# Kernel optimization log

Hardware: AMD Instinct MI355X
Metric: run time of the kernel (lower is better)

The kernel has to match this reference:

```python
import jax, jax.numpy as jnp
import numpy as np

N_NODES = 100000
N_EDGES = 1200000
D_IN = 64
D_HID = 64
BN_EPS = 1e-5


def setup_inputs() -> dict:
    key = jax.random.key(0)
    ks = jax.random.split(key, 16)
    x = jax.random.normal(ks[0], (N_NODES, D_IN), dtype=jnp.float32)
    edge_index = jax.random.randint(ks[1], (2, N_EDGES), 0, N_NODES, dtype=jnp.int64)
    s = 1.0 / np.sqrt(D_HID)
    W1 = jax.random.uniform(ks[2], (D_IN, D_HID), jnp.float32, -s, s)
    b1 = jax.random.uniform(ks[3], (D_HID,), jnp.float32, -s, s)
    W2 = jax.random.uniform(ks[4], (D_HID, D_HID), jnp.float32, -s, s)
    b2 = jax.random.uniform(ks[5], (D_HID,), jnp.float32, -s, s)
    W3 = jax.random.uniform(ks[6], (D_HID, D_HID), jnp.float32, -s, s)
    b3 = jax.random.uniform(ks[7], (D_HID,), jnp.float32, -s, s)
    gamma1 = jnp.ones((D_HID,), jnp.float32)
    beta1 = jnp.zeros((D_HID,), jnp.float32)
    gamma2 = jnp.ones((D_HID,), jnp.float32)
    beta2 = jnp.zeros((D_HID,), jnp.float32)
    return {"x": x, "edge_index": edge_index, "batch_size": 1,
            "W1": W1, "b1": b1, "gamma1": gamma1, "beta1": beta1,
            "W2": W2, "b2": b2, "gamma2": gamma2, "beta2": beta2,
            "W3": W3, "b3": b3}


def _gcn_norm(edge_index, n):
    # PyG GCNConv: add self-loops, symmetric normalization D^-1/2 (A+I) D^-1/2
    loop = jnp.arange(n, dtype=edge_index.dtype)
    src = jnp.concatenate([edge_index[0], loop])
    dst = jnp.concatenate([edge_index[1], loop])
    deg = jax.ops.segment_sum(jnp.ones_like(dst, dtype=jnp.float32), dst, num_segments=n)
    dinv = jnp.where(deg > 0, jax.lax.rsqrt(jnp.maximum(deg, 1.0)), 0.0)
    norm = dinv[src] * dinv[dst]  # [E + N]
    return src, dst, norm


def _gcn_conv(h, W, b, src, dst, norm, n):
    h = h @ W                      # [N, D]
    msg = h[src] * norm[:, None]   # gather + scale, [E+N, D]
    out = jax.ops.segment_sum(msg, dst, num_segments=n)  # scatter-add
    return out + b


def _bn_train(h, gamma, beta):
    # BatchNorm1d over nodes, training-mode (biased batch statistics)
    m = h.mean(axis=0)
    v = h.var(axis=0)
    return (h - m) * jax.lax.rsqrt(v + BN_EPS) * gamma + beta


def reference(x, edge_index, batch_size,
              W1, b1, gamma1, beta1, W2, b2, gamma2, beta2, W3, b3):
    n = x.shape[0]
    src, dst, norm = _gcn_norm(edge_index, n)
    h = _gcn_conv(x, W1, b1, src, dst, norm, n)
    h = jax.nn.relu(_bn_train(h, gamma1, beta1))
    h = _gcn_conv(h, W2, b2, src, dst, norm, n)
    h = jax.nn.relu(_bn_train(h, gamma2, beta2))
    h = _gcn_conv(h, W3, b3, src, dst, norm, n)
    return h  # output_type == 'hidden'
```

## Files before the change

kernel.cpp:

```cpp
#include <hip/hip_runtime.h>
#include <hip/hip_bf16.h>

#define D 64

typedef __attribute__((ext_vector_type(8))) short bf16x8;
typedef __attribute__((ext_vector_type(8))) unsigned short u16x8;
typedef __attribute__((ext_vector_type(4))) float f32x4;

__device__ __forceinline__ short f2bf(float x) {
    unsigned u = __float_as_uint(x);
    unsigned r = (u + 0x7fffu + ((u >> 16) & 1u)) >> 16;
    return (short)r;
}
__device__ __forceinline__ float bf2f(unsigned short u) {
    return __uint_as_float((unsigned)u << 16);
}

__global__ void detect_kernel(const unsigned int* e32, int* flag) {
    __shared__ int nz;
    if (threadIdx.x == 0) nz = 0;
    __syncthreads();
    if (e32[2 * threadIdx.x + 1] != 0) nz = 1;
    __syncthreads();
    if (threadIdx.x == 0) *flag = (nz == 0) ? 1 : 0;
}

__device__ __forceinline__ int load_idx(const void* e, int is64, long long i) {
    if (is64) return (int)((const long long*)e)[i];
    return ((const int*)e)[i];
}

#define NBLK 256

__global__ __launch_bounds__(256) void bucket_count_kernel(
    const void* edges, const int* flag, int* pbh, int E, int shift) {
    __shared__ int h[512];
    for (int i = threadIdx.x; i < 512; i += 256) h[i] = 0;
    __syncthreads();
    int is64 = *flag;
    int chunk = (E + gridDim.x - 1) / gridDim.x;
    int s0 = blockIdx.x * chunk;
    int s1 = min(E, s0 + chunk);
    for (int e = s0 + (int)threadIdx.x; e < s1; e += 256) {
        int d = load_idx(edges, is64, (long long)E + e);
        atomicAdd(&h[d >> shift], 1);
    }
    __syncthreads();
    for (int i = threadIdx.x; i < 512; i += 256) pbh[blockIdx.x * 512 + i] = h[i];
}

__global__ __launch_bounds__(256) void colscan_kernel(int* pbh, int* btot) {
    int b = blockIdx.x;
    int k = threadIdx.x;
    __shared__ int sA[256], sB[256];
    int v = pbh[k * 512 + b];
    sA[k] = v;
    __syncthreads();
    int* src = sA;
    int* dst = sB;
    for (int d = 1; d < 256; d <<= 1) {
        dst[k] = src[k] + (k >= d ? src[k - d] : 0);
        __syncthreads();
        int* t = src; src = dst; dst = t;
    }
    pbh[k * 512 + b] = src[k] - v;
    if (k == 255) btot[b] = src[255];
}

__global__ __launch_bounds__(512) void basescan_kernel(const int* btot, int* bbase, int E) {
    __shared__ int sA[512], sB[512];
    int b = threadIdx.x;
    int v = btot[b];
    sA[b] = v;
    __syncthreads();
    int* src = sA;
    int* dst = sB;
    for (int d = 1; d < 512; d <<= 1) {
        dst[b] = src[b] + (b >= d ? src[b - d] : 0);
        __syncthreads();
        int* t = src; src = dst; dst = t;
    }
    bbase[b] = src[b] - v;
    if (b == 0) bbase[512] = E;
}

__global__ __launch_bounds__(256) void bucket_scatter_kernel(
    const void* edges, const int* flag, const int* pbh, const int* bbase,
    unsigned* staging, int E, int shift) {
    __shared__ int cur[512];
    for (int i = threadIdx.x; i < 512; i += 256)
        cur[i] = pbh[blockIdx.x * 512 + i] + bbase[i];
    __syncthreads();
    int is64 = *flag;
    int chunk = (E + gridDim.x - 1) / gridDim.x;
    int s0 = blockIdx.x * chunk;
    int s1 = min(E, s0 + chunk);
    unsigned mask = (unsigned)((1 << shift) - 1);
    for (int e = s0 + (int)threadIdx.x; e < s1; e += 256) {
        int s = load_idx(edges, is64, e);
        int d = load_idx(edges, is64, (long long)E + e);
        int b = d >> shift;
        int pos = atomicAdd(&cur[b], 1);
        staging[pos] = ((unsigned)s << shift) | ((unsigned)d & mask);
    }
}

__global__ __launch_bounds__(256) void bucket_fill_kernel(
    const unsigned* __restrict__ staging, const int* __restrict__ bbase,
    int* __restrict__ offs, float* __restrict__ dinv, int* __restrict__ srcs,
    int shift, int n, int E) {
    int b = blockIdx.x;
    int bstart = bbase[b], bend = bbase[b + 1];
    int bsz = 1 << shift;
    unsigned mask = (unsigned)(bsz - 1);
    int v0 = b << shift;
    int nloc = min(bsz, n - v0);

    __shared__ int cnt[512], cur[512], sA[512], sB[512];
    for (int i = threadIdx.x; i < bsz; i += 256) cnt[i] = 0;
    __syncthreads();
    for (int idx = bstart + (int)threadIdx.x; idx < bend; idx += 256)
        atomicAdd(&cnt[staging[idx] & mask], 1);
    __syncthreads();
    for (int i = threadIdx.x; i < bsz; i += 256) sA[i] = cnt[i];
    __syncthreads();
    int* src = sA;
    int* dst = sB;
    for (int d = 1; d < bsz; d <<= 1) {
        for (int i = threadIdx.x; i < bsz; i += 256)
            dst[i] = src[i] + (i >= d ? src[i - d] : 0);
        __syncthreads();
        int* t = src; src = dst; dst = t;
    }
    for (int i = threadIdx.x; i < bsz; i += 256) {
        int excl = src[i] - cnt[i];
        cur[i] = excl;
        if (i < nloc) {
            offs[v0 + i] = bstart + excl;
            dinv[v0 + i] = rsqrtf((float)(cnt[i] + 1));
        }
    }
    if (b == 0 && threadIdx.x == 0) offs[n] = E;
    __syncthreads();
    for (int idx = bstart + (int)threadIdx.x; idx < bend; idx += 256) {
        unsigned u = staging[idx];
        int ld = (int)(u & mask);
        int pos = atomicAdd(&cur[ld], 1);
        srcs[bstart + pos] = (int)(u >> shift);
    }
}

__global__ __launch_bounds__(256) void mm_bn_kernel(
    const float* __restrict__ Xf, const unsigned short* __restrict__ Xb, int x_is_bf16,
    const float* __restrict__ W,
    const float* __restrict__ stats, const float* __restrict__ gamma,
    const float* __restrict__ beta, int use_bn, float inv_n,
    const float* __restrict__ dinv,
    unsigned short* __restrict__ Y, int n) {
    int lane = threadIdx.x & 63;
    int m = lane & 15;
    int quad = lane >> 4;

    float sc[16], sh[16];
#pragma unroll
    for (int s = 0; s < 2; s++) {
#pragma unroll
        for (int j = 0; j < 8; j++) {
            float scale = 1.f, shift = 0.f;
            if (use_bn) {
                int f = s * 32 + quad * 8 + j;
                float mean = stats[f] * inv_n;
                float var = stats[64 + f] * inv_n - mean * mean;
                float rs = rsqrtf(var + 1e-5f);
                scale = rs * gamma[f];
                shift = beta[f] - mean * scale;
            }
            sc[s * 8 + j] = scale;
            sh[s * 8 + j] = shift;
        }
    }

    bf16x8 bfrag[4][2];
#pragma unroll
    for (int nt = 0; nt < 4; nt++) {
#pragma unroll
        for (int s = 0; s < 2; s++) {
#pragma unroll
            for (int j = 0; j < 8; j++) {
                int k = s * 32 + quad * 8 + j;
                bfrag[nt][s][j] = f2bf(W[k * 64 + nt * 16 + m]);
            }
        }
    }

    int wave = blockIdx.x * 4 + (threadIdx.x >> 6);
    int nwaves = gridDim.x * 4;
    int ntiles = (n + 15) >> 4;
    const f32x4 zero = {0.f, 0.f, 0.f, 0.f};

    for (int t = wave; t < ntiles; t += nwaves) {
        int r = t * 16 + m;
        if (r >= n) r = n - 1;
        float av[16];
        if (x_is_bf16) {
            const unsigned short* xr = Xb + (long long)r * 64;
            u16x8 u0 = *(const u16x8*)(xr + quad * 8);
            u16x8 u1 = *(const u16x8*)(xr + 32 + quad * 8);
#pragma unroll
            for (int j = 0; j < 8; j++) {
                av[j] = bf2f(u0[j]);
                av[8 + j] = bf2f(u1[j]);
            }
        } else {
            const float* xr = Xf + (long long)r * 64;
            f32x4 a0 = *(const f32x4*)(xr + quad * 8);
            f32x4 a1 = *(const f32x4*)(xr + quad * 8 + 4);
            f32x4 a2 = *(const f32x4*)(xr + 32 + quad * 8);
            f32x4 a3 = *(const f32x4*)(xr + 32 + quad * 8 + 4);
#pragma unroll
            for (int j = 0; j < 4; j++) {
                av[j] = a0[j];
                av[4 + j] = a1[j];
                av[8 + j] = a2[j];
                av[12 + j] = a3[j];
            }
        }
        bf16x8 A0, A1;
#pragma unroll
        for (int j = 0; j < 8; j++) {
            float v0 = av[j] * sc[j] + sh[j];
            float v1 = av[8 + j] * sc[8 + j] + sh[8 + j];
            if (use_bn) {
                v0 = fmaxf(v0, 0.f);
                v1 = fmaxf(v1, 0.f);
            }
            A0[j] = f2bf(v0);
            A1[j] = f2bf(v1);
        }

        f32x4 acc[4];
#pragma unroll
        for (int nt = 0; nt < 4; nt++) {
            acc[nt] = __builtin_amdgcn_mfma_f32_16x16x32_bf16(A0, bfrag[nt][0], zero, 0, 0, 0);
            acc[nt] = __builtin_amdgcn_mfma_f32_16x16x32_bf16(A1, bfrag[nt][1], acc[nt], 0, 0, 0);
        }

        int row0 = t * 16 + quad * 4;
        float dv[4];
#pragma unroll
        for (int i = 0; i < 4; i++) {
            int rr = row0 + i;
            dv[i] = (rr < n) ? dinv[rr] : 0.f;
        }
#pragma unroll
        for (int nt = 0; nt < 4; nt++) {
#pragma unroll
            for (int i = 0; i < 4; i++) {
                int rr = row0 + i;
                if (rr < n)
                    Y[(long long)rr * 64 + nt * 16 + m] = (unsigned short)f2bf(acc[nt][i] * dv[i]);
            }
        }
    }
}

__global__ __launch_bounds__(256) void agg_kernel(const unsigned short* __restrict__ T,
                                                  const int* __restrict__ offs,
                                                  const int* __restrict__ srcs,
                                                  const float* __restrict__ dinv,
                                                  const float* __restrict__ bias,
                                                  unsigned short* __restrict__ out16,
                                                  float* __restrict__ out32, int out_bf16,
                                                  int n) {
    int v = blockIdx.x * 4 + (threadIdx.x >> 6);
    if (v >= n) return;
    int lane = threadIdx.x & 63;
    float acc = bf2f(T[(long long)v * D + lane]);
    int j = offs[v], j1 = offs[v + 1];
    for (; j + 8 <= j1; j += 8) {
        int sidx[8];
#pragma unroll
        for (int u = 0; u < 8; u++) sidx[u] = srcs[j + u];
        float t[8];
#pragma unroll
        for (int u = 0; u < 8; u++) t[u] = bf2f(T[(long long)sidx[u] * D + lane]);
        acc += ((t[0] + t[1]) + (t[2] + t[3])) + ((t[4] + t[5]) + (t[6] + t[7]));
    }
    if (j < j1) {
        int sidx[8];
        float wgt[8];
#pragma unroll
        for (int u = 0; u < 8; u++) {
            int jj = j + u;
            int jc = jj < j1 ? jj : j1 - 1;
            sidx[u] = srcs[jc];
            wgt[u] = (jj < j1) ? 1.f : 0.f;
        }
        float t[8];
#pragma unroll
        for (int u = 0; u < 8; u++) t[u] = bf2f(T[(long long)sidx[u] * D + lane]);
        float p0 = wgt[0] * t[0] + wgt[1] * t[1];
        float p1 = wgt[2] * t[2] + wgt[3] * t[3];
        float p2 = wgt[4] * t[4] + wgt[5] * t[5];
        float p3 = wgt[6] * t[6] + wgt[7] * t[7];
        acc += (p0 + p1) + (p2 + p3);
    }
    float val = dinv[v] * acc + bias[lane];
    if (out_bf16)
        out16[(long long)v * D + lane] = (unsigned short)f2bf(val);
    else
        out32[(long long)v * D + lane] = val;
}

__global__ __launch_bounds__(256) void bnstats_kernel(const unsigned short* __restrict__ H,
                                                      float* __restrict__ stats, int n) {
    int f = threadIdx.x & 63;
    int r = threadIdx.x >> 6;
    float s = 0.f, q = 0.f;
    for (int node = blockIdx.x * 4 + r; node < n; node += gridDim.x * 4) {
        float x = bf2f(H[(long long)node * D + f]);
        s += x;
        q += x * x;
    }
    __shared__ float ls[256], lq[256];
    ls[threadIdx.x] = s;
    lq[threadIdx.x] = q;
    __syncthreads();
    if (r == 0) {
        s = ls[f] + ls[64 + f] + ls[128 + f] + ls[192 + f];
        q = lq[f] + lq[64 + f] + lq[128 + f] + lq[192 + f];
        atomicAdd(&stats[f], s);
        atomicAdd(&stats[64 + f], q);
    }
}

extern "C" void kernel_launch(void* const* d_in, const int* in_sizes, int n_in,
                              void* d_out, int out_size, void* d_ws, size_t ws_size,
                              hipStream_t stream) {
    const float* x = (const float*)d_in[0];
    const void* edges = d_in[1];
    const float* W1 = (const float*)d_in[3];
    const float* b1 = (const float*)d_in[4];
    const float* gamma1 = (const float*)d_in[5];
    const float* beta1 = (const float*)d_in[6];
    const float* W2 = (const float*)d_in[7];
    const float* b2 = (const float*)d_in[8];
    const float* gamma2 = (const float*)d_in[9];
    const float* beta2 = (const float*)d_in[10];
    const float* W3 = (const float*)d_in[11];
    const float* b3 = (const float*)d_in[12];

    const int N = in_sizes[0] / D;
    const int E = in_sizes[1] / 2;
    const float inv_n = 1.f / (float)N;

    int shift = 8;
    while ((((long long)N - 1) >> shift) + 1 > 512) shift++;
    const int nbuk = (int)(((long long)N - 1) >> shift) + 1;

    char* ws = (char*)d_ws;
    size_t off = 0;
    auto alloc = [&](size_t bytes) -> void* {
        void* p = ws + off;
        off = (off + bytes + 255) & ~(size_t)255;
        return p;
    };
    float*    dinv    = (float*)   alloc((size_t)N * 4);
    int*      offs    = (int*)     alloc((size_t)(N + 1) * 4);
    int*      srcs    = (int*)     alloc((size_t)E * 4);
    unsigned* staging = (unsigned*)alloc((size_t)E * 4);
    int*      pbh     = (int*)     alloc((size_t)NBLK * 512 * 4);
    int*      btot    = (int*)     alloc(512 * 4);
    int*      bbase   = (int*)     alloc(513 * 4);
    int*      flag    = (int*)     alloc(4);
    float*    stats   = (float*)   alloc(256 * 4);
    unsigned short* bufA = (unsigned short*)alloc((size_t)N * D * 2);
    unsigned short* hbuf = (unsigned short*)alloc((size_t)N * D * 2);
    float*    outf    = (float*)d_out;

    const int aggb = (N + 3) / 4;

    detect_kernel<<<1, 256, 0, stream>>>((const unsigned int*)edges, flag);
    bucket_count_kernel<<<NBLK, 256, 0, stream>>>(edges, flag, pbh, E, shift);
    colscan_kernel<<<512, 256, 0, stream>>>(pbh, btot);
    basescan_kernel<<<1, 512, 0, stream>>>(btot, bbase, E);
    bucket_scatter_kernel<<<NBLK, 256, 0, stream>>>(edges, flag, pbh, bbase, staging, E, shift);
    bucket_fill_kernel<<<nbuk, 256, 0, stream>>>(staging, bbase, offs, dinv, srcs, shift, N, E);
    hipMemsetAsync(stats, 0, 256 * 4, stream);

    mm_bn_kernel<<<512, 256, 0, stream>>>(x, nullptr, 0, W1, nullptr, nullptr, nullptr, 0,
                                          inv_n, dinv, bufA, N);
    agg_kernel<<<aggb, 256, 0, stream>>>(bufA, offs, srcs, dinv, b1, hbuf, nullptr, 1, N);
    bnstats_kernel<<<512, 256, 0, stream>>>(hbuf, stats, N);

    mm_bn_kernel<<<512, 256, 0, stream>>>(nullptr, hbuf, 1, W2, stats, gamma1, beta1, 1,
                                          inv_n, dinv, bufA, N);
    agg_kernel<<<aggb, 256, 0, stream>>>(bufA, offs, srcs, dinv, b2, hbuf, nullptr, 1, N);
    bnstats_kernel<<<512, 256, 0, stream>>>(hbuf, stats + 128, N);

    mm_bn_kernel<<<512, 256, 0, stream>>>(nullptr, hbuf, 1, W3, stats + 128, gamma2, beta2, 1,
                                          inv_n, dinv, bufA, N);
    agg_kernel<<<aggb, 256, 0, stream>>>(bufA, offs, srcs, dinv, b3, nullptr, outf, 0, N);
}
```

Before: 366.2 us.

## Fuse BN statistics into vectorized grid-stride aggregation kernel

Rewrites the aggregation kernel so that each wave handles 8 nodes, and each lane loads 16-byte chunks of 8 bf16 features. Neighbor indices are shared through shuffles, and the loop is grid-strided over a fixed number of blocks. Batch-norm sums and sums of squares are accumulated in the same pass and reduced through shared and global atomics, which removes the separate bnstats kernel and its re-read of the hidden buffer. The mm grid size also changes. Padding each 8-node group to its longest neighbor list wastes some loads when degrees vary.

Measured after the change: 360.6 us. About the same (-1.5%).

```diff
diff --git a/kernel.cpp b/kernel.cpp
--- a/kernel.cpp
+++ b/kernel.cpp
@@ -264,73 +264,111 @@
     }
 }
 
-__global__ __launch_bounds__(256) void agg_kernel(const unsigned short* __restrict__ T,
-                                                  const int* __restrict__ offs,
-                                                  const int* __restrict__ srcs,
-                                                  const float* __restrict__ dinv,
-                                                  const float* __restrict__ bias,
-                                                  unsigned short* __restrict__ out16,
-                                                  float* __restrict__ out32, int out_bf16,
-                                                  int n) {
-    int v = blockIdx.x * 4 + (threadIdx.x >> 6);
-    if (v >= n) return;
+__global__ __launch_bounds__(256) void agg_kernel(
+    const unsigned short* __restrict__ T,
+    const int* __restrict__ offs,
+    const int* __restrict__ srcs,
+    const float* __restrict__ dinv,
+    const float* __restrict__ bias,
+    unsigned short* __restrict__ out16,
+    float* __restrict__ out32, int out_bf16,
+    float* __restrict__ stats, int do_stats,
+    int n, int E) {
+    __shared__ float S[128];
+    if (do_stats) {
+        if (threadIdx.x < 128) S[threadIdx.x] = 0.f;
+        __syncthreads();
+    }
     int lane = threadIdx.x & 63;
-    float acc = bf2f(T[(long long)v * D + lane]);
-    int j = offs[v], j1 = offs[v + 1];
-    for (; j + 8 <= j1; j += 8) {
-        int sidx[8];
-#pragma unroll
-        for (int u = 0; u < 8; u++) sidx[u] = srcs[j + u];
-        float t[8];
-#pragma unroll
-        for (int u = 0; u < 8; u++) t[u] = bf2f(T[(long long)sidx[u] * D + lane]);
-        acc += ((t[0] + t[1]) + (t[2] + t[3])) + ((t[4] + t[5]) + (t[6] + t[7]));
-    }
-    if (j < j1) {
-        int sidx[8];
-        float wgt[8];
-#pragma unroll
-        for (int u = 0; u < 8; u++) {
-            int jj = j + u;
-            int jc = jj < j1 ? jj : j1 - 1;
-            sidx[u] = srcs[jc];
-            wgt[u] = (jj < j1) ? 1.f : 0.f;
-        }
-        float t[8];
-#pragma unroll
-        for (int u = 0; u < 8; u++) t[u] = bf2f(T[(long long)sidx[u] * D + lane]);
-        float p0 = wgt[0] * t[0] + wgt[1] * t[1];
-        float p1 = wgt[2] * t[2] + wgt[3] * t[3];
-        float p2 = wgt[4] * t[4] + wgt[5] * t[5];
-        float p3 = wgt[6] * t[6] + wgt[7] * t[7];
-        acc += (p0 + p1) + (p2 + p3);
-    }
-    float val = dinv[v] * acc + bias[lane];
-    if (out_bf16)
-        out16[(long long)v * D + lane] = (unsigned short)f2bf(val);
-    else
-        out32[(long long)v * D + lane] = val;
-}
-
-__global__ __launch_bounds__(256) void bnstats_kernel(const unsigned short* __restrict__ H,
-                                                      float* __restrict__ stats, int n) {
-    int f = threadIdx.x & 63;
-    int r = threadIdx.x >> 6;
-    float s = 0.f, q = 0.f;
-    for (int node = blockIdx.x * 4 + r; node < n; node += gridDim.x * 4) {
-        float x = bf2f(H[(long long)node * D + f]);
-        s += x;
-        q += x * x;
-    }
-    __shared__ float ls[256], lq[256];
-    ls[threadIdx.x] = s;
-    lq[threadIdx.x] = q;
-    __syncthreads();
-    if (r == 0) {
-        s = ls[f] + ls[64 + f] + ls[128 + f] + ls[192 + f];
-        q = lq[f] + lq[64 + f] + lq[128 + f] + lq[192 + f];
-        atomicAdd(&stats[f], s);
-        atomicAdd(&stats[64 + f], q);
+    int sub = lane >> 3;
+    int c = lane & 7;
+    int wave = blockIdx.x * 4 + (threadIdx.x >> 6);
+    int nwaves = gridDim.x * 4;
+    int ngrp = (n + 7) >> 3;
+    f32x4 bi0 = *(const f32x4*)(bias + c * 8);
+    f32x4 bi1 = *(const f32x4*)(bias + c * 8 + 4);
+    float ss[8], sq[8];
+#pragma unroll
+    for (int i = 0; i < 8; i++) { ss[i] = 0.f; sq[i] = 0.f; }
+
+    for (int g = wave; g < ngrp; g += nwaves) {
+        int v = g * 8 + sub;
+        int valid = v < n;
+        int vc = valid ? v : n - 1;
+        int j0 = offs[vc];
+        int len = offs[vc + 1] - j0;
+        u16x8 sv = *(const u16x8*)(T + ((size_t)(unsigned)vc << 6) + (c << 3));
+        float acc[8];
+#pragma unroll
+        for (int i = 0; i < 8; i++) acc[i] = bf2f(sv[i]);
+        int ml = len;
+        ml = max(ml, __shfl_xor(ml, 8));
+        ml = max(ml, __shfl_xor(ml, 16));
+        ml = max(ml, __shfl_xor(ml, 32));
+        for (int base = 0; base < ml; base += 8) {
+            int my = srcs[min(j0 + base + c, E - 1)];
+            int lim = min(8, ml - base);
+            int rel = len - base;
+            for (int e = 0; e < lim; e += 4) {
+                int sid[4];
+                float w[4];
+#pragma unroll
+                for (int u = 0; u < 4; u++) {
+                    int ee = e + u;
+                    int s = __shfl(my, (lane & 56) | ee);
+                    int live = ee < rel;
+                    sid[u] = live ? s : vc;
+                    w[u] = live ? 1.f : 0.f;
+                }
+                u16x8 r[4];
+#pragma unroll
+                for (int u = 0; u < 4; u++)
+                    r[u] = *(const u16x8*)(T + ((size_t)(unsigned)sid[u] << 6) + (c << 3));
+#pragma unroll
+                for (int u = 0; u < 4; u++) {
+#pragma unroll
+                    for (int i = 0; i < 8; i++)
+                        acc[i] += w[u] * bf2f(r[u][i]);
+                }
+            }
+        }
+        float dv = dinv[vc];
+        float val[8];
+#pragma unroll
+        for (int i = 0; i < 4; i++) {
+            val[i] = dv * acc[i] + bi0[i];
+            val[4 + i] = dv * acc[4 + i] + bi1[i];
+        }
+        if (valid) {
+            if (out_bf16) {
+                u16x8 o;
+#pragma unroll
+                for (int i = 0; i < 8; i++) o[i] = (unsigned short)f2bf(val[i]);
+                *(u16x8*)(out16 + ((size_t)(unsigned)v << 6) + (c << 3)) = o;
+            } else {
+                f32x4 o0 = {val[0], val[1], val[2], val[3]};
+                f32x4 o1 = {val[4], val[5], val[6], val[7]};
+                float* op = out32 + ((size_t)(unsigned)v << 6) + (c << 3);
+                *(f32x4*)op = o0;
+                *(f32x4*)(op + 4) = o1;
+            }
+            if (do_stats) {
+#pragma unroll
+                for (int i = 0; i < 8; i++) {
+                    ss[i] += val[i];
+                    sq[i] += val[i] * val[i];
+                }
+            }
+        }
+    }
+    if (do_stats) {
+#pragma unroll
+        for (int i = 0; i < 8; i++) {
+            atomicAdd(&S[c * 8 + i], ss[i]);
+            atomicAdd(&S[64 + c * 8 + i], sq[i]);
+        }
+        __syncthreads();
+        if (threadIdx.x < 128) atomicAdd(&stats[threadIdx.x], S[threadIdx.x]);
     }
 }
 
@@ -378,7 +416,8 @@
     unsigned short* hbuf = (unsigned short*)alloc((size_t)N * D * 2);
     float*    outf    = (float*)d_out;
 
-    const int aggb = (N + 3) / 4;
+    const int AGGB = 1536;
+    const int MMB  = 782;
 
     detect_kernel<<<1, 256, 0, stream>>>((const unsigned int*)edges, flag);
     bucket_count_kernel<<<NBLK, 256, 0, stream>>>(edges, flag, pbh, E, shift);
@@ -388,17 +427,18 @@
     bucket_fill_kernel<<<nbuk, 256, 0, stream>>>(staging, bbase, offs, dinv, srcs, shift, N, E);
     hipMemsetAsync(stats, 0, 256 * 4, stream);
 
-    mm_bn_kernel<<<512, 256, 0, stream>>>(x, nullptr, 0, W1, nullptr, nullptr, nullptr, 0,
+    mm_bn_kernel<<<MMB, 256, 0, stream>>>(x, nullptr, 0, W1, nullptr, nullptr, nullptr, 0,
                                           inv_n, dinv, bufA, N);
-    agg_kernel<<<aggb, 256, 0, stream>>>(bufA, offs, srcs, dinv, b1, hbuf, nullptr, 1, N);
-    bnstats_kernel<<<512, 256, 0, stream>>>(hbuf, stats, N);
-
-    mm_bn_kernel<<<512, 256, 0, stream>>>(nullptr, hbuf, 1, W2, stats, gamma1, beta1, 1,
+    agg_kernel<<<AGGB, 256, 0, stream>>>(bufA, offs, srcs, dinv, b1, hbuf, nullptr, 1,
+                                         stats, 1, N, E);
+
+    mm_bn_kernel<<<MMB, 256, 0, stream>>>(nullptr, hbuf, 1, W2, stats, gamma1, beta1, 1,
                                           inv_n, dinv, bufA, N);
-    agg_kernel<<<aggb, 256, 0, stream>>>(bufA, offs, srcs, dinv, b2, hbuf, nullptr, 1, N);
-    bnstats_kernel<<<512, 256, 0, stream>>>(hbuf, stats + 128, N);
-
-    mm_bn_kernel<<<512, 256, 0, stream>>>(nullptr, hbuf, 1, W3, stats + 128, gamma2, beta2, 1,
+    agg_kernel<<<AGGB, 256, 0, stream>>>(bufA, offs, srcs, dinv, b2, hbuf, nullptr, 1,
+                                         stats + 128, 1, N, E);
+
+    mm_bn_kernel<<<MMB, 256, 0, stream>>>(nullptr, hbuf, 1, W3, stats + 128, gamma2, beta2, 1,
                                           inv_n, dinv, bufA, N);
-    agg_kernel<<<aggb, 256, 0, stream>>>(bufA, offs, srcs, dinv, b3, nullptr, outf, 0, N);
-}
+    agg_kernel<<<AGGB, 256, 0, stream>>>(bufA, offs, srcs, dinv, b3, nullptr, outf, 0,
+                                         nullptr, 0, N, E);
+}
```

## Fuse BatchNorm statistics into aggregation kernel with slab-based atomic reduction

Applied to the files above, without the earlier changes.

The aggregation kernel now accumulates per-feature sum and sum-of-squares of its fp32 output in shared memory. It atomically adds them into 16 slabs, and a tiny 128-thread kernel reduces the slabs. This removes the separate bnstats pass, which re-read the whole hidden buffer twice per forward. It also uses readfirstlane for the CSR bounds, switches to 32-bit index arithmetic, and changes the matmul grid size. The trade-off is roughly 25k blocks doing atomics on 16 slabs, which adds contention. The statistics now come from the unrounded fp32 values rather than the bf16-stored ones.

Result: faster. 320.8 us (-12.4%).

```diff
diff --git a/kernel.cpp b/kernel.cpp
--- a/kernel.cpp
+++ b/kernel.cpp
@@ -271,67 +271,79 @@
                                                   const float* __restrict__ bias,
                                                   unsigned short* __restrict__ out16,
                                                   float* __restrict__ out32, int out_bf16,
+                                                  float* __restrict__ slabs, int do_stats,
                                                   int n) {
     int v = blockIdx.x * 4 + (threadIdx.x >> 6);
-    if (v >= n) return;
     int lane = threadIdx.x & 63;
-    float acc = bf2f(T[(long long)v * D + lane]);
-    int j = offs[v], j1 = offs[v + 1];
-    for (; j + 8 <= j1; j += 8) {
-        int sidx[8];
-#pragma unroll
-        for (int u = 0; u < 8; u++) sidx[u] = srcs[j + u];
-        float t[8];
-#pragma unroll
-        for (int u = 0; u < 8; u++) t[u] = bf2f(T[(long long)sidx[u] * D + lane]);
-        acc += ((t[0] + t[1]) + (t[2] + t[3])) + ((t[4] + t[5]) + (t[6] + t[7]));
-    }
-    if (j < j1) {
-        int sidx[8];
-        float wgt[8];
-#pragma unroll
-        for (int u = 0; u < 8; u++) {
-            int jj = j + u;
-            int jc = jj < j1 ? jj : j1 - 1;
-            sidx[u] = srcs[jc];
-            wgt[u] = (jj < j1) ? 1.f : 0.f;
-        }
-        float t[8];
-#pragma unroll
-        for (int u = 0; u < 8; u++) t[u] = bf2f(T[(long long)sidx[u] * D + lane]);
-        float p0 = wgt[0] * t[0] + wgt[1] * t[1];
-        float p1 = wgt[2] * t[2] + wgt[3] * t[3];
-        float p2 = wgt[4] * t[4] + wgt[5] * t[5];
-        float p3 = wgt[6] * t[6] + wgt[7] * t[7];
-        acc += (p0 + p1) + (p2 + p3);
-    }
-    float val = dinv[v] * acc + bias[lane];
-    if (out_bf16)
-        out16[(long long)v * D + lane] = (unsigned short)f2bf(val);
-    else
-        out32[(long long)v * D + lane] = val;
-}
-
-__global__ __launch_bounds__(256) void bnstats_kernel(const unsigned short* __restrict__ H,
-                                                      float* __restrict__ stats, int n) {
-    int f = threadIdx.x & 63;
-    int r = threadIdx.x >> 6;
-    float s = 0.f, q = 0.f;
-    for (int node = blockIdx.x * 4 + r; node < n; node += gridDim.x * 4) {
-        float x = bf2f(H[(long long)node * D + f]);
-        s += x;
-        q += x * x;
-    }
-    __shared__ float ls[256], lq[256];
-    ls[threadIdx.x] = s;
-    lq[threadIdx.x] = q;
-    __syncthreads();
-    if (r == 0) {
-        s = ls[f] + ls[64 + f] + ls[128 + f] + ls[192 + f];
-        q = lq[f] + lq[64 + f] + lq[128 + f] + lq[192 + f];
-        atomicAdd(&stats[f], s);
-        atomicAdd(&stats[64 + f], q);
-    }
+    int valid = v < n;
+    int vc = valid ? v : n - 1;
+    float val;
+    {
+        float acc = bf2f(T[((unsigned)vc << 6) + lane]);
+        int j0 = __builtin_amdgcn_readfirstlane(offs[vc]);
+        int j1 = __builtin_amdgcn_readfirstlane(offs[vc + 1]);
+        int j = j0;
+        for (; j + 8 <= j1; j += 8) {
+            int sidx[8];
+#pragma unroll
+            for (int u = 0; u < 8; u++) sidx[u] = srcs[j + u];
+            float t[8];
+#pragma unroll
+            for (int u = 0; u < 8; u++)
+                t[u] = bf2f(T[((unsigned)sidx[u] << 6) + lane]);
+            acc += ((t[0] + t[1]) + (t[2] + t[3])) + ((t[4] + t[5]) + (t[6] + t[7]));
+        }
+        if (j < j1) {
+            int sidx[8];
+            float wgt[8];
+#pragma unroll
+            for (int u = 0; u < 8; u++) {
+                int jj = j + u;
+                int jc = jj < j1 ? jj : j1 - 1;
+                sidx[u] = srcs[jc];
+                wgt[u] = (jj < j1) ? 1.f : 0.f;
+            }
+            float t[8];
+#pragma unroll
+            for (int u = 0; u < 8; u++)
+                t[u] = bf2f(T[((unsigned)sidx[u] << 6) + lane]);
+            float p0 = wgt[0] * t[0] + wgt[1] * t[1];
+            float p1 = wgt[2] * t[2] + wgt[3] * t[3];
+            float p2 = wgt[4] * t[4] + wgt[5] * t[5];
+            float p3 = wgt[6] * t[6] + wgt[7] * t[7];
+            acc += (p0 + p1) + (p2 + p3);
+        }
+        val = dinv[vc] * acc + bias[lane];
+        if (valid) {
+            if (out_bf16)
+                out16[((unsigned)v << 6) + lane] = (unsigned short)f2bf(val);
+            else
+                out32[((unsigned)v << 6) + lane] = val;
+        }
+    }
+    if (do_stats) {
+        __shared__ float ls[256], lq[256];
+        float x = valid ? val : 0.f;
+        ls[threadIdx.x] = x;
+        lq[threadIdx.x] = x * x;
+        __syncthreads();
+        int tid = threadIdx.x;
+        if (tid < 128) {
+            int f = tid & 63;
+            const float* a = (tid < 64) ? ls : lq;
+            float r = a[f] + a[64 + f] + a[128 + f] + a[192 + f];
+            atomicAdd(&slabs[((unsigned)(blockIdx.x & 15)) * 128 + tid], r);
+        }
+    }
+}
+
+__global__ __launch_bounds__(128) void redstats_kernel(const float* __restrict__ slabs,
+                                                       float* __restrict__ out) {
+    int t = threadIdx.x;
+    float s = 0.f;
+#pragma unroll
+    for (int k = 0; k < 16; k++) s += slabs[k * 128 + t];
+    out[t] = s;
 }
 
 extern "C" void kernel_launch(void* const* d_in, const int* in_sizes, int n_in,
@@ -373,12 +385,14 @@
     int*      btot    = (int*)     alloc(512 * 4);
     int*      bbase   = (int*)     alloc(513 * 4);
     int*      flag    = (int*)     alloc(4);
-    float*    stats   = (float*)   alloc(256 * 4);
+    float*    slabs   = (float*)   alloc((size_t)2 * 16 * 128 * 4);
+    float*    canon   = (float*)   alloc(256 * 4);
     unsigned short* bufA = (unsigned short*)alloc((size_t)N * D * 2);
     unsigned short* hbuf = (unsigned short*)alloc((size_t)N * D * 2);
     float*    outf    = (float*)d_out;
 
-    const int aggb = (N + 3) / 4;
+    const int AGGB = (N + 3) / 4;
+    const int MMB  = 782;
 
     detect_kernel<<<1, 256, 0, stream>>>((const unsigned int*)edges, flag);
     bucket_count_kernel<<<NBLK, 256, 0, stream>>>(edges, flag, pbh, E, shift);
@@ -386,19 +400,22 @@
     basescan_kernel<<<1, 512, 0, stream>>>(btot, bbase, E);
     bucket_scatter_kernel<<<NBLK, 256, 0, stream>>>(edges, flag, pbh, bbase, staging, E, shift);
     bucket_fill_kernel<<<nbuk, 256, 0, stream>>>(staging, bbase, offs, dinv, srcs, shift, N, E);
-    hipMemsetAsync(stats, 0, 256 * 4, stream);
-
-    mm_bn_kernel<<<512, 256, 0, stream>>>(x, nullptr, 0, W1, nullptr, nullptr, nullptr, 0,
+    hipMemsetAsync(slabs, 0, (size_t)2 * 16 * 128 * 4, stream);
+
+    mm_bn_kernel<<<MMB, 256, 0, stream>>>(x, nullptr, 0, W1, nullptr, nullptr, nullptr, 0,
                                           inv_n, dinv, bufA, N);
-    agg_kernel<<<aggb, 256, 0, stream>>>(bufA, offs, srcs, dinv, b1, hbuf, nullptr, 1, N);
-    bnstats_kernel<<<512, 256, 0, stream>>>(hbuf, stats, N);
-
-    mm_bn_kernel<<<512, 256, 0, stream>>>(nullptr, hbuf, 1, W2, stats, gamma1, beta1, 1,
+    agg_kernel<<<AGGB, 256, 0, stream>>>(bufA, offs, srcs, dinv, b1, hbuf, nullptr, 1,
+                                         slabs, 1, N);
+    redstats_kernel<<<1, 128, 0, stream>>>(slabs, canon);
+
+    mm_bn_kernel<<<MMB, 256, 0, stream>>>(nullptr, hbuf, 1, W2, canon, gamma1, beta1, 1,
                                           inv_n, dinv, bufA, N);
-    agg_kernel<<<aggb, 256, 0, stream>>>(bufA, offs, srcs, dinv, b2, hbuf, nullptr, 1, N);
-    bnstats_kernel<<<512, 256, 0, stream>>>(hbuf, stats + 128, N);
-
-    mm_bn_kernel<<<512, 256, 0, stream>>>(nullptr, hbuf, 1, W3, stats + 128, gamma2, beta2, 1,
+    agg_kernel<<<AGGB, 256, 0, stream>>>(bufA, offs, srcs, dinv, b2, hbuf, nullptr, 1,
+                                         slabs + 16 * 128, 1, N);
+    redstats_kernel<<<1, 128, 0, stream>>>(slabs + 16 * 128, canon + 128);
+
+    mm_bn_kernel<<<MMB, 256, 0, stream>>>(nullptr, hbuf, 1, W3, canon + 128, gamma2, beta2, 1,
                                           inv_n, dinv, bufA, N);
-    agg_kernel<<<aggb, 256, 0, stream>>>(bufA, offs, srcs, dinv, b3, nullptr, outf, 0, N);
-}
+    agg_kernel<<<AGGB, 256, 0, stream>>>(bufA, offs, srcs, dinv, b3, nullptr, outf, 0,
+                                         nullptr, 0, N);
+}
```
